# Optimization experiments

Hardware: AMD Instinct MI355X
Metric: run time of the kernel (lower is better)

## Reference

```python
import jax, jax.numpy as jnp
import numpy as np

B, T, E, H = 2, 2048, 1024, 16


def setup_inputs() -> dict:
    key = jax.random.key(0)
    ks = jax.random.split(key, 6)
    s = lambda k, shape: jax.random.normal(k, shape, dtype=jnp.float32) * 0.02
    return {
        "x": jax.random.normal(ks[0], (B, T, E), dtype=jnp.float32),
        "ln1_g": jnp.ones((E,), jnp.float32),
        "ln1_b": jnp.zeros((E,), jnp.float32),
        "attn_w": s(ks[1], (E, 3 * E)),
        "attn_b": jnp.zeros((3 * E,), jnp.float32),
        "proj_w": s(ks[2], (E, E)),
        "proj_b": jnp.zeros((E,), jnp.float32),
        "ln2_g": jnp.ones((E,), jnp.float32),
        "ln2_b": jnp.zeros((E,), jnp.float32),
        "mlp_w1": s(ks[3], (E, 4 * E)),
        "mlp_b1": jnp.zeros((4 * E,), jnp.float32),
        "mlp_w2": s(ks[4], (4 * E, E)),
        "mlp_b2": jnp.zeros((E,), jnp.float32),
        "w_att": jnp.ones((1,), jnp.float32),
        "w_mlp": jnp.ones((1,), jnp.float32),
    }


def _ln(x, g, b, eps=1e-5):
    m = x.mean(-1, keepdims=True)
    v = ((x - m) ** 2).mean(-1, keepdims=True)
    return (x - m) * jax.lax.rsqrt(v + eps) * g + b


def reference(x, ln1_g, ln1_b, attn_w, attn_b, proj_w, proj_b,
              ln2_g, ln2_b, mlp_w1, mlp_b1, mlp_w2, mlp_b2, w_att, w_mlp):
    Bx, Tx, Ex = x.shape
    hd = Ex // H
    # --- self-attention on ln_1(x) ---
    qkv = _ln(x, ln1_g, ln1_b) @ attn_w + attn_b          # [B,T,3E]
    q, k, v = jnp.split(qkv, 3, axis=-1)
    q = q.reshape(Bx, Tx, H, hd)
    k = k.reshape(Bx, Tx, H, hd)
    v = v.reshape(Bx, Tx, H, hd)
    att = jnp.einsum('bthd,bshd->bhts', q, k) * (1.0 / np.sqrt(hd))  # [B,H,T,T]
    causal = jnp.tril(jnp.ones((Tx, Tx), dtype=bool))
    att = jnp.where(causal, att, -jnp.inf)
    att = jax.nn.softmax(att, axis=-1)
    y = jnp.einsum('bhts,bshd->bthd', att, v).reshape(Bx, Tx, Ex)
    y = y @ proj_w + proj_b
    x = x * w_att + y
    # --- MLP on ln_2(x) ---
    h = _ln(x, ln2_g, ln2_b) @ mlp_w1 + mlp_b1
    h = jax.nn.gelu(h, approximate=False)
    x = x * w_mlp + (h @ mlp_w2 + mlp_b2)
    return x
```

## Files before the change

### kernel.cpp

```cpp
#include <hip/hip_runtime.h>
#include <math.h>

typedef __bf16 bf16;
typedef bf16 bf16x8 __attribute__((ext_vector_type(8)));
typedef bf16 bf16x4 __attribute__((ext_vector_type(4)));
typedef float f32x4 __attribute__((ext_vector_type(4)));

#define MFMA(a, b, c) __builtin_amdgcn_mfma_f32_16x16x32_bf16((a), (b), (c), 0, 0, 0)

#define GLOAD_LDS16(gp, lp)                                                        \
  __builtin_amdgcn_global_load_lds((const __attribute__((address_space(1))) void*)(gp), \
                                   (__attribute__((address_space(3))) void*)(lp), 16, 0, 0)

static const size_t E_WT_ATTN = 0;
static const size_t E_WT_PROJ = 3145728;
static const size_t E_WT_MLP1 = 4194304;
static const size_t E_WT_MLP2 = 8388608;
static const size_t E_LN1     = 12582912;
static const size_t E_QKV     = 16777216;
static const size_t E_VT      = 37748736;
static const size_t E_Y       = 41943040;
static const size_t E_LN2     = 46137344;
static const size_t E_H       = 50331648;
static const size_t BYTE_X2    = 134217728;
static const size_t BYTE_OPART = 150994944;
static const size_t BYTE_ML    = 184549376;
static const size_t BYTE_GPART = 185597952;
static const size_t TOTAL_BYTES = 252706816;

__device__ __align__(4096) unsigned char g_buf[TOTAL_BYTES];

__global__ __launch_bounds__(256) void transpose_all(const float* __restrict__ aw,
                                                     const float* __restrict__ pw,
                                                     const float* __restrict__ m1,
                                                     const float* __restrict__ m2,
                                                     bf16* __restrict__ o_a,
                                                     bf16* __restrict__ o_p,
                                                     bf16* __restrict__ o_m1,
                                                     bf16* __restrict__ o_m2) {
  __shared__ float tile[32][33];
  int bid = blockIdx.x;
  const float* in;
  bf16* out;
  int K, N, tix;
  if (bid < 3072) { in = aw; out = o_a; K = 1024; N = 3072; tix = bid; }
  else if (bid < 4096) { in = pw; out = o_p; K = 1024; N = 1024; tix = bid - 3072; }
  else if (bid < 8192) { in = m1; out = o_m1; K = 1024; N = 4096; tix = bid - 4096; }
  else { in = m2; out = o_m2; K = 4096; N = 1024; tix = bid - 8192; }
  int ntx = N >> 5;
  int bx = tix % ntx, by = tix / ntx;
  int tx = threadIdx.x, ty = threadIdx.y;
#pragma unroll
  for (int i = ty; i < 32; i += 8)
    tile[i][tx] = in[(size_t)(by * 32 + i) * N + bx * 32 + tx];
  __syncthreads();
#pragma unroll
  for (int i = ty; i < 32; i += 8)
    out[(size_t)(bx * 32 + i) * K + by * 32 + tx] = (bf16)tile[tx][i];
}

__global__ __launch_bounds__(256) void ln_bf16(const float* __restrict__ x,
                                               const float* __restrict__ g,
                                               const float* __restrict__ b,
                                               bf16* __restrict__ out) {
  int row = blockIdx.x, tid = threadIdx.x;
  const float* xr = x + ((size_t)row << 10);
  float4 v = *(const float4*)(xr + tid * 4);
  float s = v.x + v.y + v.z + v.w;
  float ss = v.x * v.x + v.y * v.y + v.z * v.z + v.w * v.w;
#pragma unroll
  for (int off = 32; off >= 1; off >>= 1) {
    s += __shfl_down(s, off);
    ss += __shfl_down(ss, off);
  }
  __shared__ float sh[8];
  int wid = tid >> 6;
  if ((tid & 63) == 0) { sh[wid] = s; sh[wid + 4] = ss; }
  __syncthreads();
  float ts = sh[0] + sh[1] + sh[2] + sh[3];
  float tss = sh[4] + sh[5] + sh[6] + sh[7];
  float mean = ts * (1.0f / 1024.0f);
  float var = tss * (1.0f / 1024.0f) - mean * mean;
  float inv = rsqrtf(var + 1e-5f);
  float4 gg = *(const float4*)(g + tid * 4);
  float4 bb = *(const float4*)(b + tid * 4);
  bf16x4 o;
  o[0] = (bf16)((v.x - mean) * inv * gg.x + bb.x);
  o[1] = (bf16)((v.y - mean) * inv * gg.y + bb.y);
  o[2] = (bf16)((v.z - mean) * inv * gg.z + bb.z);
  o[3] = (bf16)((v.w - mean) * inv * gg.w + bb.w);
  *(bf16x4*)(out + ((size_t)row << 10) + tid * 4) = o;
}

template <int EPI>
__global__ __launch_bounds__(512, 2) void gemm256(const bf16* __restrict__ A,
                                                  const bf16* __restrict__ Bt,
                                                  const float* __restrict__ bias,
                                                  bf16* __restrict__ outb,
                                                  float* __restrict__ outf,
                                                  int M, int N, int K, int Kseg) {
  __shared__ __align__(16) bf16 As[2][16384];
  __shared__ __align__(16) bf16 Bs[2][16384];
  int tid = threadIdx.x;
  int nwg = gridDim.x * gridDim.y;
  int bid = blockIdx.y * gridDim.x + blockIdx.x;
  int id2 = ((nwg & 7) == 0) ? ((bid & 7) * (nwg >> 3) + (bid >> 3)) : bid;
  int bx = id2 % gridDim.x, by = id2 / gridDim.x;
  int lane = tid & 63, wid = tid >> 6;
  int wr = wid >> 2, wc = wid & 3;
  int g = lane >> 4, lr = lane & 15;
  f32x4 acc[8][4];
#pragma unroll
  for (int m = 0; m < 8; ++m)
#pragma unroll
    for (int n = 0; n < 4; ++n) acc[m][n] = (f32x4){0.f, 0.f, 0.f, 0.f};
  const bf16* Ab = A + (size_t)by * 256 * K;
  const bf16* Bb = Bt + (size_t)bx * 256 * K;
  int rbase = tid >> 3;
  int srccol = (((tid & 7) ^ (rbase & 7)) << 3);
  const bf16* Asrc = Ab + (size_t)rbase * K + srccol;
  const bf16* Bsrc = Bb + (size_t)rbase * K + srccol;
#define G256_STAGE(buf, k0)                                                \
  {                                                                        \
    _Pragma("unroll") for (int q = 0; q < 4; ++q) {                        \
      GLOAD_LDS16(Asrc + (size_t)(q * 64) * K + (k0), &As[buf][tid * 8 + q * 4096]); \
      GLOAD_LDS16(Bsrc + (size_t)(q * 64) * K + (k0), &Bs[buf][tid * 8 + q * 4096]); \
    }                                                                      \
  }
  int kbeg = blockIdx.z * Kseg;
  int NT = Kseg >> 6;
  G256_STAGE(0, kbeg);
  __syncthreads();
  int c = 0;
  for (int t = 0; t < NT; ++t) {
    if (t + 1 < NT) G256_STAGE(c ^ 1, kbeg + (t + 1) * 64);
#pragma unroll
    for (int kk = 0; kk < 2; ++kk) {
      bf16x8 af[8], bfv[4];
#pragma unroll
      for (int m = 0; m < 8; ++m) {
        int row = wr * 128 + m * 16 + lr;
        af[m] = *(const bf16x8*)&As[c][row * 64 + ((((kk << 2) + g) ^ (row & 7)) << 3)];
      }
#pragma unroll
      for (int n = 0; n < 4; ++n) {
        int row = wc * 64 + n * 16 + lr;
        bfv[n] = *(const bf16x8*)&Bs[c][row * 64 + ((((kk << 2) + g) ^ (row & 7)) << 3)];
      }
#pragma unroll
      for (int m = 0; m < 8; ++m)
#pragma unroll
        for (int n = 0; n < 4; ++n) acc[m][n] = MFMA(af[m], bfv[n], acc[m][n]);
    }
    __syncthreads();
    c ^= 1;
  }
#undef G256_STAGE
  if (EPI == 3) {
    float* po = outf + (size_t)blockIdx.z * M * N;
#pragma unroll
    for (int m = 0; m < 8; ++m) {
#pragma unroll
      for (int n = 0; n < 4; ++n) {
        int rg0 = by * 256 + wr * 128 + m * 16 + g * 4;
        int cg = bx * 256 + wc * 64 + n * 16 + lr;
#pragma unroll
        for (int j = 0; j < 4; ++j) po[(size_t)(rg0 + j) * N + cg] = acc[m][n][j];
      }
    }
  } else {
#pragma unroll
    for (int m = 0; m < 8; ++m) {
#pragma unroll
      for (int n = 0; n < 4; ++n) {
        int rg0 = by * 256 + wr * 128 + m * 16 + g * 4;
        int cg = bx * 256 + wc * 64 + n * 16 + lr;
        float bv = bias[cg];
#pragma unroll
        for (int j = 0; j < 4; ++j) {
          float v = acc[m][n][j] + bv;
          size_t idx = (size_t)(rg0 + j) * N + cg;
          if (EPI == 0)
            outb[idx] = (bf16)v;
          else {
            float u = 0.7978845608f * (v + 0.044715f * v * v * v);
            float e = exp2f(u * 2.885390082f);
            float th = 1.0f - 2.0f / (e + 1.0f);
            outb[idx] = (bf16)(0.5f * v * (1.0f + th));
          }
        }
      }
    }
  }
}

__global__ __launch_bounds__(256) void gemm_bt3(const bf16* __restrict__ A,
                                                const bf16* __restrict__ Bt,
                                                float* __restrict__ outf,
                                                int M, int N, int K, int Kseg) {
  __shared__ __align__(16) bf16 As[128 * 32];
  __shared__ __align__(16) bf16 Bs[128 * 32];
  int bx = blockIdx.x, by = blockIdx.y;
  int tid = threadIdx.x;
  int lane = tid & 63, wid = tid >> 6;
  int wr = wid >> 1, wc = wid & 1;
  int g = lane >> 4, lr = lane & 15;
  f32x4 acc[4][4];
#pragma unroll
  for (int m = 0; m < 4; ++m)
#pragma unroll
    for (int n = 0; n < 4; ++n) acc[m][n] = (f32x4){0.f, 0.f, 0.f, 0.f};
  const bf16* Ab = A + (size_t)by * 128 * K;
  const bf16* Bb = Bt + (size_t)bx * 128 * K;
  int srow = tid >> 2;
  int sk8 = (tid & 3) * 8;
  const bf16* Ap0 = Ab + (size_t)srow * K + sk8;
  const bf16* Ap1 = Ab + (size_t)(srow + 64) * K + sk8;
  const bf16* Bp0 = Bb + (size_t)srow * K + sk8;
  const bf16* Bp1 = Bb + (size_t)(srow + 64) * K + sk8;
  bf16* lA0 = As + tid * 8;
  bf16* lA1 = As + 2048 + tid * 8;
  bf16* lB0 = Bs + tid * 8;
  bf16* lB1 = Bs + 2048 + tid * 8;
  int kbeg = blockIdx.z * Kseg;
  int kend = kbeg + Kseg;
  for (int k0 = kbeg; k0 < kend; k0 += 32) {
    GLOAD_LDS16(Ap0 + k0, lA0);
    GLOAD_LDS16(Ap1 + k0, lA1);
    GLOAD_LDS16(Bp0 + k0, lB0);
    GLOAD_LDS16(Bp1 + k0, lB1);
    __syncthreads();
    bf16x8 af[4], bfv[4];
#pragma unroll
    for (int m = 0; m < 4; ++m) af[m] = *(const bf16x8*)(As + (wr * 64 + m * 16 + lr) * 32 + g * 8);
#pragma unroll
    for (int n = 0; n < 4; ++n) bfv[n] = *(const bf16x8*)(Bs + (wc * 64 + n * 16 + lr) * 32 + g * 8);
#pragma unroll
    for (int m = 0; m < 4; ++m)
#pragma unroll
      for (int n = 0; n < 4; ++n) acc[m][n] = MFMA(af[m], bfv[n], acc[m][n]);
    __syncthreads();
  }
  float* po = outf + (size_t)blockIdx.z * M * N;
#pragma unroll
  for (int m = 0; m < 4; ++m) {
#pragma unroll
    for (int n = 0; n < 4; ++n) {
      int rg0 = by * 128 + wr * 64 + m * 16 + g * 4;
      int cg = bx * 128 + wc * 64 + n * 16 + lr;
#pragma unroll
      for (int j = 0; j < 4; ++j) po[(size_t)(rg0 + j) * N + cg] = acc[m][n][j];
    }
  }
}

template <int SK>
__global__ __launch_bounds__(256) void reduce_add(const float* __restrict__ part,
                                                  const float* __restrict__ bias,
                                                  const float* __restrict__ res,
                                                  const float* __restrict__ wsc,
                                                  float* __restrict__ out, int MN, int N) {
  size_t i = ((size_t)blockIdx.x * 256 + threadIdx.x) * 4;
  float4 a = *(const float4*)(part + i);
#pragma unroll
  for (int s = 1; s < SK; ++s) {
    float4 b = *(const float4*)(part + (size_t)s * MN + i);
    a.x += b.x; a.y += b.y; a.z += b.z; a.w += b.w;
  }
  int col = (int)(i & (size_t)(N - 1));
  float4 bv = *(const float4*)(bias + col);
  float4 rv = *(const float4*)(res + i);
  float w = wsc[0];
  float4 o;
  o.x = rv.x * w + a.x + bv.x;
  o.y = rv.y * w + a.y + bv.y;
  o.z = rv.z * w + a.z + bv.z;
  o.w = rv.w * w + a.w + bv.w;
  *(float4*)(out + i) = o;
}

__global__ __launch_bounds__(256) void reduce_ln(const float* __restrict__ part,
                                                 const float* __restrict__ bias,
                                                 const float* __restrict__ res,
                                                 const float* __restrict__ wsc,
                                                 const float* __restrict__ lng,
                                                 const float* __restrict__ lnb,
                                                 float* __restrict__ x2out,
                                                 bf16* __restrict__ lnout) {
  int row = blockIdx.x, tid = threadIdx.x;
  size_t i = ((size_t)row << 10) + tid * 4;
  float4 a = *(const float4*)(part + i);
  float4 b2 = *(const float4*)(part + 4194304 + i);
  float4 rv = *(const float4*)(res + i);
  float4 bv = *(const float4*)(bias + tid * 4);
  float w = wsc[0];
  float4 o;
  o.x = rv.x * w + a.x + b2.x + bv.x;
  o.y = rv.y * w + a.y + b2.y + bv.y;
  o.z = rv.z * w + a.z + b2.z + bv.z;
  o.w = rv.w * w + a.w + b2.w + bv.w;
  *(float4*)(x2out + i) = o;
  float s = o.x + o.y + o.z + o.w;
  float ss = o.x * o.x + o.y * o.y + o.z * o.z + o.w * o.w;
#pragma unroll
  for (int off = 32; off >= 1; off >>= 1) {
    s += __shfl_down(s, off);
    ss += __shfl_down(ss, off);
  }
  __shared__ float sh[8];
  int wid = tid >> 6;
  if ((tid & 63) == 0) { sh[wid] = s; sh[wid + 4] = ss; }
  __syncthreads();
  float ts = sh[0] + sh[1] + sh[2] + sh[3];
  float tss = sh[4] + sh[5] + sh[6] + sh[7];
  float mean = ts * (1.0f / 1024.0f);
  float var = tss * (1.0f / 1024.0f) - mean * mean;
  float inv = rsqrtf(var + 1e-5f);
  float4 gg = *(const float4*)(lng + tid * 4);
  float4 bb = *(const float4*)(lnb + tid * 4);
  bf16x4 ov;
  ov[0] = (bf16)((o.x - mean) * inv * gg.x + bb.x);
  ov[1] = (bf16)((o.y - mean) * inv * gg.y + bb.y);
  ov[2] = (bf16)((o.z - mean) * inv * gg.z + bb.z);
  ov[3] = (bf16)((o.w - mean) * inv * gg.w + bb.w);
  *(bf16x4*)(lnout + ((size_t)row << 10) + tid * 4) = ov;
}

__global__ __launch_bounds__(256) void split_v_t(const bf16* __restrict__ qkv,
                                                 bf16* __restrict__ vT) {
  int t0 = blockIdx.x * 32;
  int bh = blockIdx.y;
  int b = bh >> 4, h = bh & 15;
  __shared__ bf16 tile[32][72];
  int tid = threadIdx.x;
  int d = tid & 63, tl0 = tid >> 6;
#pragma unroll
  for (int p = 0; p < 8; ++p) {
    int tl = p * 4 + tl0;
    tile[tl][d] = qkv[((size_t)(b * 2048 + t0 + tl)) * 3072 + 2048 + h * 64 + d];
  }
  __syncthreads();
  int tl = tid & 31, dq = tid >> 5;
#pragma unroll
  for (int p = 0; p < 8; ++p) {
    int dd = p * 8 + dq;
    vT[((size_t)(bh * 64 + dd)) * 2048 + t0 + tl] = tile[tl][dd];
  }
}

__global__ __launch_bounds__(256) void attn_fwd(const bf16* __restrict__ qkv,
                                                const bf16* __restrict__ vT,
                                                float* __restrict__ o_part,
                                                float* __restrict__ ml_part) {
  __shared__ __align__(16) bf16 Ks[2][4096];
  __shared__ __align__(16) bf16 Vs[2][4096];
  __shared__ bf16 P[4][16][72];
  int id = blockIdx.x;
  int bh = id & 31;
  int seg = (id >> 5) & 1;
  int qi = ((id >> 6) + bh) & 31;
  int tid = threadIdx.x, wid = tid >> 6, lane = tid & 63;
  int g = lane >> 4, lr = lane & 15;
  int b = bh >> 4, h = bh & 15;
  int nk = qi + 1;
  int n0 = (nk + 1) >> 1;
  int kt0 = seg ? n0 : 0;
  int kt1 = seg ? nk : n0;
  int qrow = qi * 64 + wid * 16 + lr;
  const bf16* Qr = qkv + ((size_t)(b * 2048 + qrow)) * 3072 + h * 64;
  const float beta = 0.18033688f;
  bf16x8 qf[2];
  qf[0] = *(const bf16x8*)(Qr + g * 8);
  qf[1] = *(const bf16x8*)(Qr + 32 + g * 8);
#pragma unroll
  for (int kk = 0; kk < 2; ++kk)
#pragma unroll
    for (int e = 0; e < 8; ++e) qf[kk][e] = (bf16)((float)qf[kk][e] * beta);
  int r0 = tid >> 3, cs0 = ((tid & 7) ^ (r0 & 7)) << 3;
  int c1i = tid + 256;
  int r1 = c1i >> 3, cs1 = ((c1i & 7) ^ (r1 & 7)) << 3;
  const bf16* sK0 = qkv + ((size_t)(b * 2048 + r0)) * 3072 + 1024 + h * 64 + cs0;
  const bf16* sK1 = qkv + ((size_t)(b * 2048 + r1)) * 3072 + 1024 + h * 64 + cs1;
  const bf16* sV0 = vT + (size_t)bh * 131072 + (size_t)r0 * 2048 + cs0;
  const bf16* sV1 = vT + (size_t)bh * 131072 + (size_t)r1 * 2048 + cs1;
  bf16* dK0 = &Ks[0][0] + tid * 8;
  bf16* dK1 = &Ks[0][0] + 2048 + tid * 8;
  bf16* dV0 = &Vs[0][0] + tid * 8;
  bf16* dV1 = &Vs[0][0] + 2048 + tid * 8;
#define ATTN_STAGE(bufsel, ktv)                          \
  {                                                      \
    size_t kadv = (size_t)(ktv) * (64 * 3072);           \
    size_t vadv = (size_t)(ktv) * 64;                    \
    int bo = (bufsel) * 4096;                            \
    GLOAD_LDS16(sK0 + kadv, dK0 + bo);                   \
    GLOAD_LDS16(sK1 + kadv, dK1 + bo);                   \
    GLOAD_LDS16(sV0 + vadv, dV0 + bo);                   \
    GLOAD_LDS16(sV1 + vadv, dV1 + bo);                   \
  }
  f32x4 o[4];
#pragma unroll
  for (int n = 0; n < 4; ++n) o[n] = (f32x4){0.f, 0.f, 0.f, 0.f};
  float m = -3e38f, l = 0.f;
  if (kt0 < kt1) ATTN_STAGE(0, kt0);
  __syncthreads();
  int sw = lr & 7;
  int sb = (lane & 48) | (g << 2);
  for (int kt = kt0; kt < kt1; ++kt) {
    int cur = (kt - kt0) & 1;
    if (kt + 1 < kt1) ATTN_STAGE(cur ^ 1, kt + 1);
    const bf16* Kb = &Ks[cur][0];
    const bf16* Vb = &Vs[cur][0];
    f32x4 s[4];
#pragma unroll
    for (int n = 0; n < 4; ++n) s[n] = (f32x4){0.f, 0.f, 0.f, 0.f};
#pragma unroll
    for (int kk = 0; kk < 2; ++kk) {
#pragma unroll
      for (int n = 0; n < 4; ++n) {
        bf16x8 kf = *(const bf16x8*)(Kb + ((n * 16 + lr) << 6) + ((((kk << 2) + g) ^ sw) << 3));
        s[n] = MFMA(kf, qf[kk], s[n]);
      }
    }
    if (kt == qi) {
      int kc0 = kt * 64 + g * 4;
#pragma unroll
      for (int n = 0; n < 4; ++n)
#pragma unroll
        for (int j = 0; j < 4; ++j)
          if ((kc0 + n * 16 + j) > qrow) s[n][j] = -3e38f;
    }
    float mx = s[0][0];
#pragma unroll
    for (int n = 0; n < 4; ++n)
#pragma unroll
      for (int j = 0; j < 4; ++j) mx = fmaxf(mx, s[n][j]);
    mx = fmaxf(mx, __shfl_xor(mx, 16));
    mx = fmaxf(mx, __shfl_xor(mx, 32));
    bool defer = __all(mx <= m + 11.5416f);
    float mn = m, al = 0.f;
    if (!defer) {
      mn = fmaxf(m, mx);
      al = exp2f(m - mn);
      m = mn;
    }
    float rs = 0.f;
    bf16x4 pw[4];
#pragma unroll
    for (int n = 0; n < 4; ++n)
#pragma unroll
      for (int j = 0; j < 4; ++j) {
        float p = exp2f(s[n][j] - mn);
        rs += p;
        pw[n][j] = (bf16)p;
      }
    rs += __shfl_xor(rs, 16);
    rs += __shfl_xor(rs, 32);
    if (defer) {
      l += rs;
    } else {
      l = l * al + rs;
      float alj[4];
#pragma unroll
      for (int j = 0; j < 4; ++j) alj[j] = __shfl(al, sb + j);
#pragma unroll
      for (int n = 0; n < 4; ++n)
#pragma unroll
        for (int j = 0; j < 4; ++j) o[n][j] *= alj[j];
    }
#pragma unroll
    for (int n = 0; n < 4; ++n) *(bf16x4*)&P[wid][lr][n * 16 + g * 4] = pw[n];
#pragma unroll
    for (int kk = 0; kk < 2; ++kk) {
      bf16x8 pf = *(const bf16x8*)&P[wid][lr][kk * 32 + g * 8];
#pragma unroll
      for (int n = 0; n < 4; ++n) {
        bf16x8 vf = *(const bf16x8*)(Vb + ((n * 16 + lr) << 6) + ((((kk << 2) + g) ^ sw) << 3));
        o[n] = MFMA(pf, vf, o[n]);
      }
    }
    __syncthreads();
  }
  float* ob = o_part + (size_t)id * 4096;
#pragma unroll
  for (int n = 0; n < 4; ++n)
#pragma unroll
    for (int j = 0; j < 4; ++j)
      ob[(size_t)(wid * 16 + g * 4 + j) * 64 + n * 16 + lr] = o[n][j];
  if (lane < 16) {
    ml_part[(size_t)id * 128 + (wid * 16 + lane) * 2] = m;
    ml_part[(size_t)id * 128 + (wid * 16 + lane) * 2 + 1] = l;
  }
#undef ATTN_STAGE
}

__global__ __launch_bounds__(256) void attn_combine(const float* __restrict__ o_part,
                                                    const float* __restrict__ ml_part,
                                                    bf16* __restrict__ y) {
  int c = blockIdx.x;
  int bh = c & 31, qi = c >> 5;
  int b = bh >> 4, h = bh & 15;
  int qraw = (qi - bh) & 31;
  size_t id0 = (size_t)bh + ((size_t)qraw << 6);
  size_t id1 = id0 + 32;
  int t = threadIdx.x;
  int r = t >> 2, cq = (t & 3) << 4;
  float m1 = ml_part[id0 * 128 + r * 2], l1 = ml_part[id0 * 128 + r * 2 + 1];
  float m2 = ml_part[id1 * 128 + r * 2], l2 = ml_part[id1 * 128 + r * 2 + 1];
  float mm = fmaxf(m1, m2);
  float w1 = exp2f(m1 - mm), w2 = exp2f(m2 - mm);
  float inv = 1.0f / (l1 * w1 + l2 * w2);
  const float* p1 = o_part + id0 * 4096 + r * 64 + cq;
  const float* p2 = o_part + id1 * 4096 + r * 64 + cq;
  bf16* yp = y + ((size_t)(b * 2048 + qi * 64 + r)) * 1024 + h * 64 + cq;
#pragma unroll
  for (int u = 0; u < 4; ++u) {
    float4 a = *(const float4*)(p1 + u * 4);
    float4 bq = *(const float4*)(p2 + u * 4);
    bf16x4 ov;
    ov[0] = (bf16)((a.x * w1 + bq.x * w2) * inv);
    ov[1] = (bf16)((a.y * w1 + bq.y * w2) * inv);
    ov[2] = (bf16)((a.z * w1 + bq.z * w2) * inv);
    ov[3] = (bf16)((a.w * w1 + bq.w * w2) * inv);
    *(bf16x4*)(yp + u * 4) = ov;
  }
}

extern "C" void kernel_launch(void* const* d_in, const int* in_sizes, int n_in,
                              void* d_out, int out_size, void* d_ws, size_t ws_size,
                              hipStream_t stream) {
  const float* x = (const float*)d_in[0];
  const float* ln1_g = (const float*)d_in[1];
  const float* ln1_b = (const float*)d_in[2];
  const float* attn_w = (const float*)d_in[3];
  const float* attn_b = (const float*)d_in[4];
  const float* proj_w = (const float*)d_in[5];
  const float* proj_b = (const float*)d_in[6];
  const float* ln2_g = (const float*)d_in[7];
  const float* ln2_b = (const float*)d_in[8];
  const float* mlp_w1 = (const float*)d_in[9];
  const float* mlp_b1 = (const float*)d_in[10];
  const float* mlp_w2 = (const float*)d_in[11];
  const float* mlp_b2 = (const float*)d_in[12];
  const float* w_att = (const float*)d_in[13];
  const float* w_mlp = (const float*)d_in[14];
  float* out = (float*)d_out;

  unsigned char* base = nullptr;
  if (ws_size >= TOTAL_BYTES) {
    base = (unsigned char*)d_ws;
  } else {
    hipGetSymbolAddress((void**)&base, HIP_SYMBOL(g_buf));
  }
  bf16* bb = (bf16*)base;
  bf16* wt_attn = bb + E_WT_ATTN;
  bf16* wt_proj = bb + E_WT_PROJ;
  bf16* wt_mlp1 = bb + E_WT_MLP1;
  bf16* wt_mlp2 = bb + E_WT_MLP2;
  bf16* ln1o = bb + E_LN1;
  bf16* qkv = bb + E_QKV;
  bf16* vTb = bb + E_VT;
  bf16* yb = bb + E_Y;
  bf16* ln2o = bb + E_LN2;
  bf16* hb = bb + E_H;
  float* x2 = (float*)(base + BYTE_X2);
  float* o_part = (float*)(base + BYTE_OPART);
  float* ml_part = (float*)(base + BYTE_ML);
  float* gpart = (float*)(base + BYTE_GPART);

  transpose_all<<<12288, dim3(32, 8), 0, stream>>>(attn_w, proj_w, mlp_w1, mlp_w2,
                                                   wt_attn, wt_proj, wt_mlp1, wt_mlp2);

  ln_bf16<<<4096, 256, 0, stream>>>(x, ln1_g, ln1_b, ln1o);

  gemm256<0><<<dim3(12, 16, 1), 512, 0, stream>>>(ln1o, wt_attn, attn_b, qkv, nullptr,
                                                  4096, 3072, 1024, 1024);

  split_v_t<<<dim3(64, 32), 256, 0, stream>>>(qkv, vTb);

  attn_fwd<<<2048, 256, 0, stream>>>(qkv, vTb, o_part, ml_part);
  attn_combine<<<1024, 256, 0, stream>>>(o_part, ml_part, yb);

  gemm_bt3<<<dim3(8, 32, 2), 256, 0, stream>>>(yb, wt_proj, gpart, 4096, 1024, 1024, 512);
  reduce_ln<<<4096, 256, 0, stream>>>(gpart, proj_b, x, w_att, ln2_g, ln2_b, x2, ln2o);

  gemm256<1><<<dim3(16, 16, 1), 512, 0, stream>>>(ln2o, wt_mlp1, mlp_b1, hb, nullptr,
                                                  4096, 4096, 1024, 1024);

  gemm256<3><<<dim3(4, 16, 4), 512, 0, stream>>>(hb, wt_mlp2, nullptr, nullptr, gpart,
                                                 4096, 1024, 4096, 1024);
  reduce_add<4><<<4096, 256, 0, stream>>>(gpart, mlp_b2, x2, w_mlp, out, 4194304, 1024);
}
```

Measured before the change: 385.2 us.

## Deepen GEMM pipeline with two-stage prefetch and fine-grained vmcnt waits

Rewrites the 256x256 GEMM main loop to keep two global-to-LDS stages in flight. It loads all LDS fragments for both k-halves up front, issues the first half of the MFMAs, then barriers and refills the just-consumed buffer for tile t+2 while the second half of the MFMAs runs. Full __syncthreads are replaced with explicit vmcnt/lgkmcnt waits plus s_barrier, so the wait covers only the older stage. This is meant to hide global load latency better, at the cost of more live registers (both fragment sets) and fragile hand-placed waitcnt counts.

```diff
diff --git a/kernel.cpp b/kernel.cpp
--- a/kernel.cpp
+++ b/kernel.cpp
@@ -130,29 +130,48 @@
   int kbeg = blockIdx.z * Kseg;
   int NT = Kseg >> 6;
   G256_STAGE(0, kbeg);
-  __syncthreads();
+  if (NT > 1) {
+    G256_STAGE(1, kbeg + 64);
+    asm volatile("s_waitcnt vmcnt(8)" ::: "memory");
+  } else {
+    asm volatile("s_waitcnt vmcnt(0)" ::: "memory");
+  }
+  __builtin_amdgcn_sched_barrier(0);
+  __builtin_amdgcn_s_barrier();
   int c = 0;
   for (int t = 0; t < NT; ++t) {
-    if (t + 1 < NT) G256_STAGE(c ^ 1, kbeg + (t + 1) * 64);
-#pragma unroll
-    for (int kk = 0; kk < 2; ++kk) {
-      bf16x8 af[8], bfv[4];
-#pragma unroll
-      for (int m = 0; m < 8; ++m) {
-        int row = wr * 128 + m * 16 + lr;
-        af[m] = *(const bf16x8*)&As[c][row * 64 + ((((kk << 2) + g) ^ (row & 7)) << 3)];
-      }
-#pragma unroll
-      for (int n = 0; n < 4; ++n) {
-        int row = wc * 64 + n * 16 + lr;
-        bfv[n] = *(const bf16x8*)&Bs[c][row * 64 + ((((kk << 2) + g) ^ (row & 7)) << 3)];
-      }
-#pragma unroll
-      for (int m = 0; m < 8; ++m)
-#pragma unroll
-        for (int n = 0; n < 4; ++n) acc[m][n] = MFMA(af[m], bfv[n], acc[m][n]);
-    }
-    __syncthreads();
+    bf16x8 a0[8], b0[4], a1[8], b1[4];
+#pragma unroll
+    for (int m = 0; m < 8; ++m) {
+      int row = wr * 128 + m * 16 + lr;
+      a0[m] = *(const bf16x8*)&As[c][row * 64 + ((g ^ (row & 7)) << 3)];
+      a1[m] = *(const bf16x8*)&As[c][row * 64 + (((4 + g) ^ (row & 7)) << 3)];
+    }
+#pragma unroll
+    for (int n = 0; n < 4; ++n) {
+      int row = wc * 64 + n * 16 + lr;
+      b0[n] = *(const bf16x8*)&Bs[c][row * 64 + ((g ^ (row & 7)) << 3)];
+      b1[n] = *(const bf16x8*)&Bs[c][row * 64 + (((4 + g) ^ (row & 7)) << 3)];
+    }
+#pragma unroll
+    for (int m = 0; m < 8; ++m)
+#pragma unroll
+      for (int n = 0; n < 4; ++n) acc[m][n] = MFMA(a0[m], b0[n], acc[m][n]);
+    asm volatile("s_waitcnt lgkmcnt(0)" ::: "memory");
+    __builtin_amdgcn_sched_barrier(0);
+    __builtin_amdgcn_s_barrier();
+    if (t + 2 < NT) G256_STAGE(c, kbeg + (t + 2) * 64);
+#pragma unroll
+    for (int m = 0; m < 8; ++m)
+#pragma unroll
+      for (int n = 0; n < 4; ++n) acc[m][n] = MFMA(a1[m], b1[n], acc[m][n]);
+    if (t + 2 < NT) {
+      asm volatile("s_waitcnt vmcnt(8)" ::: "memory");
+    } else if (t + 1 < NT) {
+      asm volatile("s_waitcnt vmcnt(0)" ::: "memory");
+    }
+    __builtin_amdgcn_sched_barrier(0);
+    __builtin_amdgcn_s_barrier();
     c ^= 1;
   }
 #undef G256_STAGE
```

After: 373.9 us. -2.9%, faster.
